# Performance work log

Measured on AMD Instinct MI355X. Metric: run time of the kernel, lower is better.

## Reference

```python
import jax, jax.numpy as jnp
import numpy as np

B, N1, N2 = 8, 2048, 2048
K1D, K2D, V1D, V2D, AD = 256, 256, 256, 256, 128


def setup_inputs() -> dict:
    key = jax.random.key(0)
    ks = jax.random.split(key, 8)
    scale1 = 1.0 / np.sqrt(K1D)
    scale2 = 1.0 / np.sqrt(K2D)
    return {
        "k1": jax.random.normal(ks[0], (B, N1, K1D), jnp.float32),
        "k2": jax.random.normal(ks[1], (B, N2, K2D), jnp.float32),
        "v1": jax.random.normal(ks[2], (B, N1, V1D), jnp.float32),
        "v2": jax.random.normal(ks[3], (B, N2, V2D), jnp.float32),
        "W1": jax.random.uniform(ks[4], (K1D, AD), jnp.float32, -scale1, scale1),
        "b1": jax.random.uniform(ks[5], (AD,), jnp.float32, -scale1, scale1),
        "W2": jax.random.uniform(ks[6], (K2D, AD), jnp.float32, -scale2, scale2),
        "b2": jax.random.uniform(ks[7], (AD,), jnp.float32, -scale2, scale2),
    }


def reference(k1, k2, v1, v2, W1, b1, W2, b2):
    k1p = k1 @ W1 + b1                      # [B, N1, A]
    k2p = k2 @ W2 + b2                      # [B, N2, A]
    score = jnp.einsum("bnd,bmd->bnm", k1p, k2p)   # [B, N1, N2]
    w1 = jax.nn.softmax(score, axis=1)      # softmax over N1 == softmax(score^T, -1)^T
    w2 = jax.nn.softmax(score, axis=-1)     # [B, N1, N2]
    o1 = jnp.einsum("bnm,bnd->bmd", w1, v1)  # [B, N2, V1D]
    o2 = jnp.einsum("bnm,bmd->bnd", w2, v2)  # [B, N1, V2D]
    return (o2, o1)
```

## Files before the change

### kernel.cpp

```cpp
#include <hip/hip_runtime.h>
#include <hip/hip_bf16.h>

#define B_  8
#define N_  2048
#define KD_ 256
#define AD_ 128
#define VD_ 256
#define SQL2E 1.2011224087864498f

using s16x8 = __attribute__((ext_vector_type(8))) short;
using f16x8 = __attribute__((ext_vector_type(8))) _Float16;
using h2    = __attribute__((ext_vector_type(2))) __fp16;
using f32x4 = __attribute__((ext_vector_type(4))) float;

__device__ __forceinline__ f32x4 mfma16(s16x8 a, s16x8 b, f32x4 c) {
  return __builtin_amdgcn_mfma_f32_16x16x32_f16(
      __builtin_bit_cast(f16x8, a), __builtin_bit_cast(f16x8, b), c, 0, 0, 0);
}
__device__ __forceinline__ short f2h(float f) {
  _Float16 h = (_Float16)f;
  return *reinterpret_cast<short*>(&h);
}
__device__ __forceinline__ float exp2_hw(float x) {
#if __has_builtin(__builtin_amdgcn_exp2f)
  return __builtin_amdgcn_exp2f(x);
#else
  float r;
  asm volatile("v_exp_f32 %0, %1" : "=v"(r) : "v"(x));
  return r;
#endif
}
__device__ __forceinline__ s16x8 cvt8(const float* __restrict__ p) {
  union { s16x8 v; h2 h[4]; } u;
  f32x4 a = *(const f32x4*)p;
  f32x4 bq = *(const f32x4*)(p + 4);
  u.h[0] = __builtin_amdgcn_cvt_pkrtz(a[0], a[1]);
  u.h[1] = __builtin_amdgcn_cvt_pkrtz(a[2], a[3]);
  u.h[2] = __builtin_amdgcn_cvt_pkrtz(bq[0], bq[1]);
  u.h[3] = __builtin_amdgcn_cvt_pkrtz(bq[2], bq[3]);
  return u.v;
}

__global__ __launch_bounds__(256) void prep_k(
    const float* __restrict__ k1, const float* __restrict__ k2,
    const float* __restrict__ v1, const float* __restrict__ v2,
    const float* __restrict__ W1, const float* __restrict__ b1f,
    const float* __restrict__ W2, const float* __restrict__ b2f,
    short* __restrict__ q1p, short* __restrict__ q2p,
    short* __restrict__ vt1, short* __restrict__ vt2) {
  __shared__ __align__(16) short sWT[128 * 264];
  const int t  = threadIdx.x;
  const int id = blockIdx.x;

  if (id < 512) {
    const int kt = id & 31, b = (id >> 5) & 7, z = id >> 8;
    const float* src = z ? v2 : v1;
    short*       dst = z ? vt2 : vt1;
    const size_t base = ((size_t)(b * 32 + kt)) * (256 * 64);
    const int w = t >> 6, vchunk = (t >> 4) & 3, l16 = t & 15;
    #pragma unroll
    for (int i = 0; i < 8; i++) {
      float x[8];
      #pragma unroll
      for (int kk = 0; kk < 8; kk++)
        x[kk] = src[((size_t)(b * N_ + kt * 64 + i * 8 + kk)) * VD_ + t];
      union { s16x8 v; h2 h[4]; } u;
      #pragma unroll
      for (int kk = 0; kk < 4; kk++)
        u.h[kk] = __builtin_amdgcn_cvt_pkrtz(x[2 * kk], x[2 * kk + 1]);
      int f = vchunk * 2 + (i >> 2);
      *(s16x8*)&dst[base + (size_t)((w * 8 + f) * 64 + (i & 3) * 16 + l16) * 8] = u.v;
    }
    return;
  }

  const int pid = id - 512;
  const int z = pid >> 8, mb = pid & 255;
  const float* X    = z ? k2 : k1;
  const float* W    = z ? W2 : W1;
  const float* bias = z ? b2f : b1f;
  short*       Y    = z ? q2p : q1p;
  const int m0   = mb * 64;
  const int lane = t & 63, wave = t >> 6, quad = lane >> 4, l16 = lane & 15;

  #pragma unroll
  for (int j = 0; j < 64; j++) {
    int idx = j * 256 + t;
    int n = idx & 127, kh = idx >> 7;
    h2 p = __builtin_amdgcn_cvt_pkrtz(W[(size_t)(2 * kh) * AD_ + n] * SQL2E,
                                      W[(size_t)(2 * kh + 1) * AD_ + n] * SQL2E);
    *(h2*)&sWT[n * 264 + kh * 2] = p;
  }
  const float* xrow = &X[(size_t)(m0 + wave * 16 + l16) * KD_];
  s16x8 a[8];
  #pragma unroll
  for (int ks = 0; ks < 8; ks++) a[ks] = cvt8(xrow + ks * 32 + quad * 8);
  __syncthreads();

  f32x4 acc[8];
  #pragma unroll
  for (int nt = 0; nt < 8; nt++) acc[nt] = (f32x4){0.f, 0.f, 0.f, 0.f};
  #pragma unroll
  for (int ks = 0; ks < 8; ks++) {
    #pragma unroll
    for (int nt = 0; nt < 8; nt++) {
      s16x8 bf = *(const s16x8*)&sWT[(nt * 16 + l16) * 264 + ks * 32 + quad * 8];
      acc[nt] = mfma16(a[ks], bf, acc[nt]);
    }
  }
  #pragma unroll
  for (int nt = 0; nt < 8; nt++) {
    float bv = bias[nt * 16 + l16] * SQL2E;
    #pragma unroll
    for (int r = 0; r < 4; r++) {
      int row = m0 + wave * 16 + quad * 4 + r;
      Y[(size_t)row * AD_ + nt * 16 + l16] = f2h(acc[nt][r] + bv);
    }
  }
}

__global__ __launch_bounds__(256, 2) void attn_k(
    const short* __restrict__ q1p, const short* __restrict__ q2p,
    const short* __restrict__ vt1, const short* __restrict__ vt2,
    float* __restrict__ out) {
  __shared__ __align__(16) short sK[2][64 * 136];
  __shared__ __align__(16) short sP[2][4][16 * 64];
  __shared__ __align__(16) float sAl[2][68];

  const int t    = threadIdx.x;
  const int lane = t & 63, wave = t >> 6, quad = lane >> 4, l16 = lane & 15;
  const int id   = blockIdx.x;
  const int xcd  = id & 7, seq = id >> 3;
  const int bp   = xcd * 2 + (seq >> 5);
  const int qb   = seq & 31;
  const int b    = bp & 7, pass = bp >> 3;
  const int q0   = qb * 64;
  const short* Q  = pass ? q2p : q1p;
  const short* K  = pass ? q1p : q2p;
  const short* Vt = pass ? vt1 : vt2;
  float* O = out + (size_t)pass * ((size_t)B_ * N_ * VD_);

  const short* kp = K + (size_t)(b * N_) * AD_ + (size_t)(t >> 4) * AD_ + (t & 15) * 8;
  const short* vp = Vt + (size_t)b * 32 * (256 * 64) + wave * 4096 + lane * 8;

  s16x8 qf[4];
  #pragma unroll
  for (int ks = 0; ks < 4; ks++)
    qf[ks] = *(const s16x8*)&Q[((size_t)(b * N_ + q0 + wave * 16 + l16)) * AD_ +
                               ks * 32 + quad * 8];

  float m_i = -1e30f, l_i = 0.f;
  f32x4 acc[16];
  #pragma unroll
  for (int c0 = 0; c0 < 16; c0++) acc[c0] = (f32x4){0.f, 0.f, 0.f, 0.f};

  s16x8 pk[4], pv[8];
  auto loadK = [&]() {
    #pragma unroll
    for (int i = 0; i < 4; i++) pk[i] = *(const s16x8*)(kp + i * 16 * AD_);
    kp += 64 * AD_;
  };
  auto loadV = [&]() {
    #pragma unroll
    for (int f = 0; f < 8; f++) pv[f] = *(const s16x8*)(vp + f * 512);
    vp += 256 * 64;
  };
  auto storeK = [&](int cb) {
    #pragma unroll
    for (int i = 0; i < 4; i++) {
      int chunk = i * 256 + t, row = chunk >> 4, c8 = chunk & 15;
      *(s16x8*)&sK[cb][row * 136 + c8 * 8] = pk[i];
    }
  };

  loadK(); storeK(0); loadK(); loadV();
  __syncthreads();

  int c = 0;
  for (int kt = 0; kt < 32; kt++) {
    f32x4 st[4];
    #pragma unroll
    for (int nt = 0; nt < 4; nt++) st[nt] = (f32x4){0.f, 0.f, 0.f, 0.f};
    __builtin_amdgcn_s_setprio(1);
    #pragma unroll
    for (int ks = 0; ks < 4; ks++) {
      #pragma unroll
      for (int nt = 0; nt < 4; nt++) {
        s16x8 kf = *(const s16x8*)&sK[c][(nt * 16 + l16) * 136 + ks * 32 + quad * 8];
        st[nt] = mfma16(kf, qf[ks], st[nt]);
      }
    }
    __builtin_amdgcn_s_setprio(0);

    float c0 = fmaxf(fmaxf(st[0][0], st[1][0]), fmaxf(st[2][0], st[3][0]));
    float c1 = fmaxf(fmaxf(st[0][1], st[1][1]), fmaxf(st[2][1], st[3][1]));
    float c2 = fmaxf(fmaxf(st[0][2], st[1][2]), fmaxf(st[2][2], st[3][2]));
    float c3 = fmaxf(fmaxf(st[0][3], st[1][3]), fmaxf(st[2][3], st[3][3]));
    float mt = fmaxf(fmaxf(c0, c1), fmaxf(c2, c3));
    mt = fmaxf(mt, __shfl_xor(mt, 16));
    mt = fmaxf(mt, __shfl_xor(mt, 32));

    float alpha = 1.f;
    bool  resc  = !__all(mt - m_i <= 8.f);
    if (resc) {
      float mn = fmaxf(m_i, mt);
      alpha = exp2_hw(m_i - mn);
      l_i *= alpha;
      m_i  = mn;
    }

    f32x4 psv = (f32x4){0.f, 0.f, 0.f, 0.f};
    #pragma unroll
    for (int nt = 0; nt < 4; nt++) {
      #pragma unroll
      for (int r = 0; r < 4; r++) {
        float p = exp2_hw(st[nt][r] - m_i);
        st[nt][r] = p;
        psv[r] += p;
      }
    }
    l_i += (psv[0] + psv[1]) + (psv[2] + psv[3]);

    #pragma unroll
    for (int nt = 0; nt < 4; nt++) {
      union { h2 h[2]; uint2 u; } wu;
      wu.h[0] = __builtin_amdgcn_cvt_pkrtz(st[nt][0], st[nt][1]);
      wu.h[1] = __builtin_amdgcn_cvt_pkrtz(st[nt][2], st[nt][3]);
      int cp = (nt * 4 + quad) ^ ((l16 & 7) << 1);
      *(uint2*)&sP[c][wave][l16 * 64 + cp * 4] = wu.u;
    }
    if (quad == 0) sAl[c][wave * 16 + l16] = alpha;
    if (lane == 0) sAl[c][64 + wave] = resc ? 1.f : 0.f;

    if (kt + 1 < 32) storeK(1 - c);

    __syncthreads();

    if (kt + 2 < 32) loadK();

    f32x4 fl = *(const f32x4*)&sAl[c][64];
    if (fl[0] + fl[1] + fl[2] + fl[3] != 0.f) {
      #pragma unroll
      for (int m = 0; m < 4; m++) {
        f32x4 aR = *(const f32x4*)&sAl[c][m * 16 + quad * 4];
        #pragma unroll
        for (int v = 0; v < 4; v++) {
          #pragma unroll
          for (int r = 0; r < 4; r++) acc[m * 4 + v][r] *= aR[r];
        }
      }
    }

    __builtin_amdgcn_s_setprio(1);
    #pragma unroll
    for (int m = 0; m < 4; m++) {
      #pragma unroll
      for (int ks2 = 0; ks2 < 2; ks2++) {
        int cp = (ks2 * 8 + quad * 2) ^ ((l16 & 7) << 1);
        s16x8 af = *(const s16x8*)&sP[c][m][l16 * 64 + cp * 4];
        #pragma unroll
        for (int v = 0; v < 4; v++)
          acc[m * 4 + v] = mfma16(af, pv[v * 2 + ks2], acc[m * 4 + v]);
      }
    }
    __builtin_amdgcn_s_setprio(0);

    if (kt + 1 < 32) loadV();
    c ^= 1;
  }

  float lf = l_i + __shfl_xor(l_i, 16);
  lf += __shfl_xor(lf, 32);
  if (quad == 0) sAl[0][wave * 16 + l16] = lf;
  __syncthreads();
  #pragma unroll
  for (int m = 0; m < 4; m++) {
    f32x4 lv = *(const f32x4*)&sAl[0][m * 16 + quad * 4];
    #pragma unroll
    for (int r = 0; r < 4; r++) {
      float inv = 1.f / lv[r];
      int row = q0 + m * 16 + quad * 4 + r;
      #pragma unroll
      for (int v = 0; v < 4; v++)
        O[((size_t)(b * N_ + row)) * VD_ + wave * 64 + v * 16 + l16] =
            acc[m * 4 + v][r] * inv;
    }
  }
}

extern "C" void kernel_launch(void* const* d_in, const int* in_sizes, int n_in,
                              void* d_out, int out_size, void* d_ws, size_t ws_size,
                              hipStream_t stream) {
  const float* k1 = (const float*)d_in[0];
  const float* k2 = (const float*)d_in[1];
  const float* v1 = (const float*)d_in[2];
  const float* v2 = (const float*)d_in[3];
  const float* W1 = (const float*)d_in[4];
  const float* b1 = (const float*)d_in[5];
  const float* W2 = (const float*)d_in[6];
  const float* b2 = (const float*)d_in[7];

  short* ws  = (short*)d_ws;
  short* q1p = ws;
  short* q2p = q1p + (size_t)16384 * 128;
  short* vt1 = q2p + (size_t)16384 * 128;
  short* vt2 = vt1 + (size_t)B_ * 32 * 256 * 64;
  float* out = (float*)d_out;

  prep_k<<<dim3(1024), dim3(256), 0, stream>>>(k1, k2, v1, v2, W1, b1, W2, b2,
                                               q1p, q2p, vt1, vt2);
  attn_k<<<dim3(512), dim3(256), 0, stream>>>(q1p, q2p, vt1, vt2, out);
}
```

Measured before the change: 180.9 us.

## Halve query tile to 32 rows and split key block across wave pairs

Each block now handles 32 query rows instead of 64, launching twice as many blocks. The four waves are split into two query halves and two key halves, and the row max is exchanged through shared memory. P is shared so each wave accumulates over all 64 keys for half the value columns. Fewer accumulator registers allow launch_bounds of 4 blocks per CU, aiming for higher occupancy. The cost is an extra barrier per iteration, more shared-memory traffic, and K/V tiles being reloaded by twice as many blocks.

New measurement: 219.4 us. +21.3%, slower.

```diff
diff --git a/kernel.cpp b/kernel.cpp
--- a/kernel.cpp
+++ b/kernel.cpp
@@ -119,22 +119,25 @@
   }
 }
 
-__global__ __launch_bounds__(256, 2) void attn_k(
+__global__ __launch_bounds__(256, 4) void attn_k(
     const short* __restrict__ q1p, const short* __restrict__ q2p,
     const short* __restrict__ vt1, const short* __restrict__ vt2,
     float* __restrict__ out) {
   __shared__ __align__(16) short sK[2][64 * 136];
-  __shared__ __align__(16) short sP[2][4][16 * 64];
-  __shared__ __align__(16) float sAl[2][68];
+  __shared__ __align__(16) short sP[4][16 * 40];
+  __shared__ __align__(16) float sM[64];
+  __shared__ __align__(16) float sAl[32];
+  __shared__ __align__(16) float sFl[4];
 
   const int t    = threadIdx.x;
   const int lane = t & 63, wave = t >> 6, quad = lane >> 4, l16 = lane & 15;
+  const int qh   = wave & 1, kh = wave >> 1;
   const int id   = blockIdx.x;
   const int xcd  = id & 7, seq = id >> 3;
-  const int bp   = xcd * 2 + (seq >> 5);
-  const int qb   = seq & 31;
+  const int bp   = xcd * 2 + (seq >> 6);
+  const int qb   = seq & 63;
   const int b    = bp & 7, pass = bp >> 3;
-  const int q0   = qb * 64;
+  const int q0   = qb * 32;
   const short* Q  = pass ? q2p : q1p;
   const short* K  = pass ? q1p : q2p;
   const short* Vt = pass ? vt1 : vt2;
@@ -146,13 +149,13 @@
   s16x8 qf[4];
   #pragma unroll
   for (int ks = 0; ks < 4; ks++)
-    qf[ks] = *(const s16x8*)&Q[((size_t)(b * N_ + q0 + wave * 16 + l16)) * AD_ +
+    qf[ks] = *(const s16x8*)&Q[((size_t)(b * N_ + q0 + qh * 16 + l16)) * AD_ +
                                ks * 32 + quad * 8];
 
   float m_i = -1e30f, l_i = 0.f;
-  f32x4 acc[16];
-  #pragma unroll
-  for (int c0 = 0; c0 < 16; c0++) acc[c0] = (f32x4){0.f, 0.f, 0.f, 0.f};
+  f32x4 acc[8];
+  #pragma unroll
+  for (int c0 = 0; c0 < 8; c0++) acc[c0] = (f32x4){0.f, 0.f, 0.f, 0.f};
 
   s16x8 pk[4], pv[8];
   auto loadK = [&]() {
@@ -176,30 +179,36 @@
   loadK(); storeK(0); loadK(); loadV();
   __syncthreads();
 
-  int c = 0;
   for (int kt = 0; kt < 32; kt++) {
-    f32x4 st[4];
-    #pragma unroll
-    for (int nt = 0; nt < 4; nt++) st[nt] = (f32x4){0.f, 0.f, 0.f, 0.f};
+    const int c = kt & 1;
+    f32x4 st[2];
+    st[0] = (f32x4){0.f, 0.f, 0.f, 0.f};
+    st[1] = (f32x4){0.f, 0.f, 0.f, 0.f};
     __builtin_amdgcn_s_setprio(1);
     #pragma unroll
     for (int ks = 0; ks < 4; ks++) {
       #pragma unroll
-      for (int nt = 0; nt < 4; nt++) {
-        s16x8 kf = *(const s16x8*)&sK[c][(nt * 16 + l16) * 136 + ks * 32 + quad * 8];
+      for (int nt = 0; nt < 2; nt++) {
+        s16x8 kf = *(const s16x8*)&sK[c][(kh * 32 + nt * 16 + l16) * 136 +
+                                         ks * 32 + quad * 8];
         st[nt] = mfma16(kf, qf[ks], st[nt]);
       }
     }
     __builtin_amdgcn_s_setprio(0);
 
-    float c0 = fmaxf(fmaxf(st[0][0], st[1][0]), fmaxf(st[2][0], st[3][0]));
-    float c1 = fmaxf(fmaxf(st[0][1], st[1][1]), fmaxf(st[2][1], st[3][1]));
-    float c2 = fmaxf(fmaxf(st[0][2], st[1][2]), fmaxf(st[2][2], st[3][2]));
-    float c3 = fmaxf(fmaxf(st[0][3], st[1][3]), fmaxf(st[2][3], st[3][3]));
-    float mt = fmaxf(fmaxf(c0, c1), fmaxf(c2, c3));
-    mt = fmaxf(mt, __shfl_xor(mt, 16));
-    mt = fmaxf(mt, __shfl_xor(mt, 32));
-
+    float a0 = fmaxf(st[0][0], st[1][0]), a1 = fmaxf(st[0][1], st[1][1]);
+    float a2 = fmaxf(st[0][2], st[1][2]), a3 = fmaxf(st[0][3], st[1][3]);
+    float hm = fmaxf(fmaxf(a0, a1), fmaxf(a2, a3));
+    hm = fmaxf(hm, __shfl_xor(hm, 16));
+    hm = fmaxf(hm, __shfl_xor(hm, 32));
+    if (quad == 0) sM[wave * 16 + l16] = hm;
+
+    if (kt + 1 < 32) storeK(1 - c);
+    __syncthreads();
+    if (kt + 2 < 32) loadK();
+
+    float pm = sM[(wave ^ 2) * 16 + l16];
+    float mt = fmaxf(hm, pm);
     float alpha = 1.f;
     bool  resc  = !__all(mt - m_i <= 8.f);
     if (resc) {
@@ -208,10 +217,9 @@
       l_i *= alpha;
       m_i  = mn;
     }
-
     f32x4 psv = (f32x4){0.f, 0.f, 0.f, 0.f};
     #pragma unroll
-    for (int nt = 0; nt < 4; nt++) {
+    for (int nt = 0; nt < 2; nt++) {
       #pragma unroll
       for (int r = 0; r < 4; r++) {
         float p = exp2_hw(st[nt][r] - m_i);
@@ -222,27 +230,22 @@
     l_i += (psv[0] + psv[1]) + (psv[2] + psv[3]);
 
     #pragma unroll
-    for (int nt = 0; nt < 4; nt++) {
+    for (int nt = 0; nt < 2; nt++) {
       union { h2 h[2]; uint2 u; } wu;
       wu.h[0] = __builtin_amdgcn_cvt_pkrtz(st[nt][0], st[nt][1]);
       wu.h[1] = __builtin_amdgcn_cvt_pkrtz(st[nt][2], st[nt][3]);
-      int cp = (nt * 4 + quad) ^ ((l16 & 7) << 1);
-      *(uint2*)&sP[c][wave][l16 * 64 + cp * 4] = wu.u;
-    }
-    if (quad == 0) sAl[c][wave * 16 + l16] = alpha;
-    if (lane == 0) sAl[c][64 + wave] = resc ? 1.f : 0.f;
-
-    if (kt + 1 < 32) storeK(1 - c);
-
+      int cpw = (nt * 4 + quad) ^ ((l16 & 3) << 1);
+      *(uint2*)&sP[wave][l16 * 40 + cpw * 4] = wu.u;
+    }
+    if (wave < 2 && quad == 0) sAl[wave * 16 + l16] = alpha;
+    if (wave < 2 && lane == 0) sFl[wave] = resc ? 1.f : 0.f;
     __syncthreads();
 
-    if (kt + 2 < 32) loadK();
-
-    f32x4 fl = *(const f32x4*)&sAl[c][64];
-    if (fl[0] + fl[1] + fl[2] + fl[3] != 0.f) {
-      #pragma unroll
-      for (int m = 0; m < 4; m++) {
-        f32x4 aR = *(const f32x4*)&sAl[c][m * 16 + quad * 4];
+    float f0 = sFl[0], f1 = sFl[1];
+    if (f0 + f1 != 0.f) {
+      #pragma unroll
+      for (int m = 0; m < 2; m++) {
+        f32x4 aR = *(const f32x4*)&sAl[m * 16 + quad * 4];
         #pragma unroll
         for (int v = 0; v < 4; v++) {
           #pragma unroll
@@ -253,11 +256,11 @@
 
     __builtin_amdgcn_s_setprio(1);
     #pragma unroll
-    for (int m = 0; m < 4; m++) {
+    for (int m = 0; m < 2; m++) {
       #pragma unroll
       for (int ks2 = 0; ks2 < 2; ks2++) {
-        int cp = (ks2 * 8 + quad * 2) ^ ((l16 & 7) << 1);
-        s16x8 af = *(const s16x8*)&sP[c][m][l16 * 64 + cp * 4];
+        int cp = (2 * quad) ^ ((l16 & 3) << 1);
+        s16x8 af = *(const s16x8*)&sP[ks2 * 2 + m][l16 * 40 + cp * 4];
         #pragma unroll
         for (int v = 0; v < 4; v++)
           acc[m * 4 + v] = mfma16(af, pv[v * 2 + ks2], acc[m * 4 + v]);
@@ -266,16 +269,18 @@
     __builtin_amdgcn_s_setprio(0);
 
     if (kt + 1 < 32) loadV();
-    c ^= 1;
   }
 
   float lf = l_i + __shfl_xor(l_i, 16);
   lf += __shfl_xor(lf, 32);
-  if (quad == 0) sAl[0][wave * 16 + l16] = lf;
+  if (quad == 0) sM[wave * 16 + l16] = lf;
   __syncthreads();
-  #pragma unroll
-  for (int m = 0; m < 4; m++) {
-    f32x4 lv = *(const f32x4*)&sAl[0][m * 16 + quad * 4];
+  if (wave < 2 && quad == 0)
+    sAl[wave * 16 + l16] = sM[wave * 16 + l16] + sM[(wave + 2) * 16 + l16];
+  __syncthreads();
+  #pragma unroll
+  for (int m = 0; m < 2; m++) {
+    f32x4 lv = *(const f32x4*)&sAl[m * 16 + quad * 4];
     #pragma unroll
     for (int r = 0; r < 4; r++) {
       float inv = 1.f / lv[r];
@@ -309,5 +314,5 @@
 
   prep_k<<<dim3(1024), dim3(256), 0, stream>>>(k1, k2, v1, v2, W1, b1, W2, b2,
                                                q1p, q2p, vt1, vt2);
-  attn_k<<<dim3(512), dim3(256), 0, stream>>>(q1p, q2p, vt1, vt2, out);
-}
+  attn_k<<<dim3(1024), dim3(256), 0, stream>>>(q1p, q2p, vt1, vt2, out);
+}
```

## Split QK^T over key columns per wave and software-pipeline PV across iterations

Applied to the files above, without the earlier changes.

Each wave now loads its own 16-key slice of K straight from global memory into registers and computes scores for all 64 queries, so the shared K tile and its staging stores go away. Row maxima are combined across waves through a small shared buffer. The P·V step for iteration i-1 is deferred and overlapped with the QK^T of iteration i behind a single barrier per iteration. In exchange, each wave holds four times as many Q fragments in registers, does a cross-wave max reduction, and the rescale decision is made per block instead of per wave, which raises register pressure and may hurt occupancy.

Result: no change. 180.6 us, median of 2 (-0.2%).

```diff
diff --git a/kernel.cpp b/kernel.cpp
--- a/kernel.cpp
+++ b/kernel.cpp
@@ -123,9 +123,10 @@
     const short* __restrict__ q1p, const short* __restrict__ q2p,
     const short* __restrict__ vt1, const short* __restrict__ vt2,
     float* __restrict__ out) {
-  __shared__ __align__(16) short sK[2][64 * 136];
-  __shared__ __align__(16) short sP[2][4][16 * 64];
-  __shared__ __align__(16) float sAl[2][68];
+  __shared__ __align__(16) short sP[2][64 * 64];
+  __shared__ __align__(16) float sMt[2][4][16][4];
+  __shared__ __align__(16) float sAl[2][64];
+  __shared__ __align__(16) float sL[64];
 
   const int t    = threadIdx.x;
   const int lane = t & 63, wave = t >> 6, quad = lane >> 4, l16 = lane & 15;
@@ -140,24 +141,27 @@
   const short* Vt = pass ? vt1 : vt2;
   float* O = out + (size_t)pass * ((size_t)B_ * N_ * VD_);
 
-  const short* kp = K + (size_t)(b * N_) * AD_ + (size_t)(t >> 4) * AD_ + (t & 15) * 8;
+  const short* kp = K + ((size_t)(b * N_) + wave * 16 + l16) * AD_ + quad * 8;
   const short* vp = Vt + (size_t)b * 32 * (256 * 64) + wave * 4096 + lane * 8;
 
-  s16x8 qf[4];
-  #pragma unroll
-  for (int ks = 0; ks < 4; ks++)
-    qf[ks] = *(const s16x8*)&Q[((size_t)(b * N_ + q0 + wave * 16 + l16)) * AD_ +
-                               ks * 32 + quad * 8];
-
-  float m_i = -1e30f, l_i = 0.f;
+  s16x8 qf[4][4];
+  #pragma unroll
+  for (int qt = 0; qt < 4; qt++)
+    #pragma unroll
+    for (int ks = 0; ks < 4; ks++)
+      qf[qt][ks] = *(const s16x8*)&Q[((size_t)(b * N_ + q0 + qt * 16 + l16)) * AD_ +
+                                     ks * 32 + quad * 8];
+
+  f32x4 m4 = (f32x4){-1e30f, -1e30f, -1e30f, -1e30f};
+  f32x4 l4 = (f32x4){0.f, 0.f, 0.f, 0.f};
   f32x4 acc[16];
   #pragma unroll
   for (int c0 = 0; c0 < 16; c0++) acc[c0] = (f32x4){0.f, 0.f, 0.f, 0.f};
 
-  s16x8 pk[4], pv[8];
+  s16x8 kf[4], pv[8];
   auto loadK = [&]() {
     #pragma unroll
-    for (int i = 0; i < 4; i++) pk[i] = *(const s16x8*)(kp + i * 16 * AD_);
+    for (int ks = 0; ks < 4; ks++) kf[ks] = *(const s16x8*)(kp + ks * 32);
     kp += 64 * AD_;
   };
   auto loadV = [&]() {
@@ -165,125 +169,145 @@
     for (int f = 0; f < 8; f++) pv[f] = *(const s16x8*)(vp + f * 512);
     vp += 256 * 64;
   };
-  auto storeK = [&](int cb) {
-    #pragma unroll
-    for (int i = 0; i < 4; i++) {
-      int chunk = i * 256 + t, row = chunk >> 4, c8 = chunk & 15;
-      *(s16x8*)&sK[cb][row * 136 + c8 * 8] = pk[i];
-    }
-  };
-
-  loadK(); storeK(0); loadK(); loadV();
+
+  loadK();
+  loadV();
+
+  f32x4 stq[4];
+  bool prevResc = false;
+
+  for (int i = 0; i <= 32; i++) {
+    const int c = i & 1;
+    if (i < 32) {
+      #pragma unroll
+      for (int qt = 0; qt < 4; qt++) stq[qt] = (f32x4){0.f, 0.f, 0.f, 0.f};
+      __builtin_amdgcn_s_setprio(1);
+      #pragma unroll
+      for (int ks = 0; ks < 4; ks++) {
+        #pragma unroll
+        for (int qt = 0; qt < 4; qt++)
+          stq[qt] = mfma16(kf[ks], qf[qt][ks], stq[qt]);
+      }
+      __builtin_amdgcn_s_setprio(0);
+
+      float hm0 = fmaxf(fmaxf(stq[0][0], stq[0][1]), fmaxf(stq[0][2], stq[0][3]));
+      float hm1 = fmaxf(fmaxf(stq[1][0], stq[1][1]), fmaxf(stq[1][2], stq[1][3]));
+      float hm2 = fmaxf(fmaxf(stq[2][0], stq[2][1]), fmaxf(stq[2][2], stq[2][3]));
+      float hm3 = fmaxf(fmaxf(stq[3][0], stq[3][1]), fmaxf(stq[3][2], stq[3][3]));
+      hm0 = fmaxf(hm0, __shfl_xor(hm0, 16)); hm0 = fmaxf(hm0, __shfl_xor(hm0, 32));
+      hm1 = fmaxf(hm1, __shfl_xor(hm1, 16)); hm1 = fmaxf(hm1, __shfl_xor(hm1, 32));
+      hm2 = fmaxf(hm2, __shfl_xor(hm2, 16)); hm2 = fmaxf(hm2, __shfl_xor(hm2, 32));
+      hm3 = fmaxf(hm3, __shfl_xor(hm3, 16)); hm3 = fmaxf(hm3, __shfl_xor(hm3, 32));
+      if (quad == 0) {
+        f32x4 hv = (f32x4){hm0, hm1, hm2, hm3};
+        *(f32x4*)&sMt[c][wave][l16][0] = hv;
+      }
+    }
+
+    __syncthreads();
+    if (i + 1 < 32) loadK();
+
+    if (i > 0) {
+      const int cprev = 1 - c;
+      if (prevResc) {
+        #pragma unroll
+        for (int m = 0; m < 4; m++) {
+          f32x4 aR = *(const f32x4*)&sAl[cprev][m * 16 + quad * 4];
+          #pragma unroll
+          for (int v = 0; v < 4; v++) {
+            #pragma unroll
+            for (int r = 0; r < 4; r++) acc[m * 4 + v][r] *= aR[r];
+          }
+        }
+      }
+      __builtin_amdgcn_s_setprio(1);
+      #pragma unroll
+      for (int m = 0; m < 4; m++) {
+        #pragma unroll
+        for (int ks2 = 0; ks2 < 2; ks2++) {
+          int physr = (ks2 * 8 + quad * 2) ^ ((l16 & 7) << 1);
+          s16x8 af = *(const s16x8*)&sP[cprev][(m * 16 + l16) * 64 + physr * 4];
+          #pragma unroll
+          for (int v = 0; v < 4; v++)
+            acc[m * 4 + v] = mfma16(af, pv[v * 2 + ks2], acc[m * 4 + v]);
+        }
+      }
+      __builtin_amdgcn_s_setprio(0);
+      if (i < 32) loadV();
+    }
+
+    if (i < 32) {
+      f32x4 w0 = *(const f32x4*)&sMt[c][0][l16][0];
+      f32x4 w1 = *(const f32x4*)&sMt[c][1][l16][0];
+      f32x4 w2 = *(const f32x4*)&sMt[c][2][l16][0];
+      f32x4 w3 = *(const f32x4*)&sMt[c][3][l16][0];
+      f32x4 mt4;
+      #pragma unroll
+      for (int qt = 0; qt < 4; qt++)
+        mt4[qt] = fmaxf(fmaxf(w0[qt], w1[qt]), fmaxf(w2[qt], w3[qt]));
+
+      bool ok = (mt4[0] - m4[0] <= 8.f) && (mt4[1] - m4[1] <= 8.f) &&
+                (mt4[2] - m4[2] <= 8.f) && (mt4[3] - m4[3] <= 8.f);
+      bool resc = !__all(ok);
+      if (resc) {
+        f32x4 al;
+        #pragma unroll
+        for (int qt = 0; qt < 4; qt++) {
+          float mn = fmaxf(m4[qt], mt4[qt]);
+          al[qt]  = exp2_hw(m4[qt] - mn);
+          m4[qt]  = mn;
+          l4[qt] *= al[qt];
+        }
+        if (wave == 0 && quad == 0) {
+          #pragma unroll
+          for (int qt = 0; qt < 4; qt++) sAl[c][qt * 16 + l16] = al[qt];
+        }
+      }
+      prevResc = resc;
+
+      #pragma unroll
+      for (int qt = 0; qt < 4; qt++) {
+        float p0 = exp2_hw(stq[qt][0] - m4[qt]);
+        float p1 = exp2_hw(stq[qt][1] - m4[qt]);
+        float p2 = exp2_hw(stq[qt][2] - m4[qt]);
+        float p3 = exp2_hw(stq[qt][3] - m4[qt]);
+        l4[qt] += (p0 + p1) + (p2 + p3);
+        union { h2 h[2]; uint2 u; } wu;
+        wu.h[0] = __builtin_amdgcn_cvt_pkrtz(p0, p1);
+        wu.h[1] = __builtin_amdgcn_cvt_pkrtz(p2, p3);
+        int phys = (wave * 4 + quad) ^ ((l16 & 7) << 1);
+        *(uint2*)&sP[c][(qt * 16 + l16) * 64 + phys * 4] = wu.u;
+      }
+    }
+  }
+
+  #pragma unroll
+  for (int qt = 0; qt < 4; qt++) {
+    l4[qt] += __shfl_xor(l4[qt], 16);
+    l4[qt] += __shfl_xor(l4[qt], 32);
+  }
+  if (quad == 0) *(f32x4*)&sMt[0][wave][l16][0] = l4;
   __syncthreads();
-
-  int c = 0;
-  for (int kt = 0; kt < 32; kt++) {
-    f32x4 st[4];
-    #pragma unroll
-    for (int nt = 0; nt < 4; nt++) st[nt] = (f32x4){0.f, 0.f, 0.f, 0.f};
-    __builtin_amdgcn_s_setprio(1);
-    #pragma unroll
-    for (int ks = 0; ks < 4; ks++) {
-      #pragma unroll
-      for (int nt = 0; nt < 4; nt++) {
-        s16x8 kf = *(const s16x8*)&sK[c][(nt * 16 + l16) * 136 + ks * 32 + quad * 8];
-        st[nt] = mfma16(kf, qf[ks], st[nt]);
-      }
-    }
-    __builtin_amdgcn_s_setprio(0);
-
-    float c0 = fmaxf(fmaxf(st[0][0], st[1][0]), fmaxf(st[2][0], st[3][0]));
-    float c1 = fmaxf(fmaxf(st[0][1], st[1][1]), fmaxf(st[2][1], st[3][1]));
-    float c2 = fmaxf(fmaxf(st[0][2], st[1][2]), fmaxf(st[2][2], st[3][2]));
-    float c3 = fmaxf(fmaxf(st[0][3], st[1][3]), fmaxf(st[2][3], st[3][3]));
-    float mt = fmaxf(fmaxf(c0, c1), fmaxf(c2, c3));
-    mt = fmaxf(mt, __shfl_xor(mt, 16));
-    mt = fmaxf(mt, __shfl_xor(mt, 32));
-
-    float alpha = 1.f;
-    bool  resc  = !__all(mt - m_i <= 8.f);
-    if (resc) {
-      float mn = fmaxf(m_i, mt);
-      alpha = exp2_hw(m_i - mn);
-      l_i *= alpha;
-      m_i  = mn;
-    }
-
-    f32x4 psv = (f32x4){0.f, 0.f, 0.f, 0.f};
-    #pragma unroll
-    for (int nt = 0; nt < 4; nt++) {
-      #pragma unroll
-      for (int r = 0; r < 4; r++) {
-        float p = exp2_hw(st[nt][r] - m_i);
-        st[nt][r] = p;
-        psv[r] += p;
-      }
-    }
-    l_i += (psv[0] + psv[1]) + (psv[2] + psv[3]);
-
-    #pragma unroll
-    for (int nt = 0; nt < 4; nt++) {
-      union { h2 h[2]; uint2 u; } wu;
-      wu.h[0] = __builtin_amdgcn_cvt_pkrtz(st[nt][0], st[nt][1]);
-      wu.h[1] = __builtin_amdgcn_cvt_pkrtz(st[nt][2], st[nt][3]);
-      int cp = (nt * 4 + quad) ^ ((l16 & 7) << 1);
-      *(uint2*)&sP[c][wave][l16 * 64 + cp * 4] = wu.u;
-    }
-    if (quad == 0) sAl[c][wave * 16 + l16] = alpha;
-    if (lane == 0) sAl[c][64 + wave] = resc ? 1.f : 0.f;
-
-    if (kt + 1 < 32) storeK(1 - c);
-
-    __syncthreads();
-
-    if (kt + 2 < 32) loadK();
-
-    f32x4 fl = *(const f32x4*)&sAl[c][64];
-    if (fl[0] + fl[1] + fl[2] + fl[3] != 0.f) {
-      #pragma unroll
-      for (int m = 0; m < 4; m++) {
-        f32x4 aR = *(const f32x4*)&sAl[c][m * 16 + quad * 4];
-        #pragma unroll
-        for (int v = 0; v < 4; v++) {
-          #pragma unroll
-          for (int r = 0; r < 4; r++) acc[m * 4 + v][r] *= aR[r];
-        }
-      }
-    }
-
-    __builtin_amdgcn_s_setprio(1);
-    #pragma unroll
-    for (int m = 0; m < 4; m++) {
-      #pragma unroll
-      for (int ks2 = 0; ks2 < 2; ks2++) {
-        int cp = (ks2 * 8 + quad * 2) ^ ((l16 & 7) << 1);
-        s16x8 af = *(const s16x8*)&sP[c][m][l16 * 64 + cp * 4];
-        #pragma unroll
-        for (int v = 0; v < 4; v++)
-          acc[m * 4 + v] = mfma16(af, pv[v * 2 + ks2], acc[m * 4 + v]);
-      }
-    }
-    __builtin_amdgcn_s_setprio(0);
-
-    if (kt + 1 < 32) loadV();
-    c ^= 1;
-  }
-
-  float lf = l_i + __shfl_xor(l_i, 16);
-  lf += __shfl_xor(lf, 32);
-  if (quad == 0) sAl[0][wave * 16 + l16] = lf;
+  if (wave == 0 && quad == 0) {
+    f32x4 s0 = *(const f32x4*)&sMt[0][0][l16][0];
+    f32x4 s1 = *(const f32x4*)&sMt[0][1][l16][0];
+    f32x4 s2 = *(const f32x4*)&sMt[0][2][l16][0];
+    f32x4 s3 = *(const f32x4*)&sMt[0][3][l16][0];
+    #pragma unroll
+    for (int qt = 0; qt < 4; qt++)
+      sL[qt * 16 + l16] = 1.f / (s0[qt] + s1[qt] + s2[qt] + s3[qt]);
+  }
   __syncthreads();
   #pragma unroll
   for (int m = 0; m < 4; m++) {
-    f32x4 lv = *(const f32x4*)&sAl[0][m * 16 + quad * 4];
+    f32x4 lv = *(const f32x4*)&sL[m * 16 + quad * 4];
     #pragma unroll
     for (int r = 0; r < 4; r++) {
-      float inv = 1.f / lv[r];
       int row = q0 + m * 16 + quad * 4 + r;
       #pragma unroll
       for (int v = 0; v < 4; v++)
         O[((size_t)(b * N_ + row)) * VD_ + wave * 64 + v * 16 + l16] =
-            acc[m * 4 + v][r] * inv;
+            acc[m * 4 + v][r] * lv[r];
     }
   }
 }
```

## Load K fragments directly from global into registers, dropping LDS staging

Applied to the files above, without the earlier changes.

Removes the shared-memory double buffer for the K tile. Each wave now loads its full set of MFMA K fragments (16 x 8 halves per lane) straight from global memory into registers, prefetching the next tile right after the QK MFMAs. This cuts the LDS store/read traffic and its bank pressure. The cost is that every wave fetches the whole K tile redundantly (4x global/L2 reads) and register pressure rises by 64 VGPRs, which could hurt occupancy at launch_bounds(256,2).

Result: slower. 254.4 us (+40.7%).

```diff
diff --git a/kernel.cpp b/kernel.cpp
--- a/kernel.cpp
+++ b/kernel.cpp
@@ -123,7 +123,6 @@
     const short* __restrict__ q1p, const short* __restrict__ q2p,
     const short* __restrict__ vt1, const short* __restrict__ vt2,
     float* __restrict__ out) {
-  __shared__ __align__(16) short sK[2][64 * 136];
   __shared__ __align__(16) short sP[2][4][16 * 64];
   __shared__ __align__(16) float sAl[2][68];
 
@@ -140,7 +139,7 @@
   const short* Vt = pass ? vt1 : vt2;
   float* O = out + (size_t)pass * ((size_t)B_ * N_ * VD_);
 
-  const short* kp = K + (size_t)(b * N_) * AD_ + (size_t)(t >> 4) * AD_ + (t & 15) * 8;
+  const short* kp = K + ((size_t)(b * N_) + l16) * AD_ + quad * 8;
   const short* vp = Vt + (size_t)b * 32 * (256 * 64) + wave * 4096 + lane * 8;
 
   s16x8 qf[4];
@@ -154,10 +153,13 @@
   #pragma unroll
   for (int c0 = 0; c0 < 16; c0++) acc[c0] = (f32x4){0.f, 0.f, 0.f, 0.f};
 
-  s16x8 pk[4], pv[8];
-  auto loadK = [&]() {
-    #pragma unroll
-    for (int i = 0; i < 4; i++) pk[i] = *(const s16x8*)(kp + i * 16 * AD_);
+  s16x8 kf[16], pv[8];
+  auto loadK16 = [&]() {
+    #pragma unroll
+    for (int x = 0; x < 16; x++) {
+      int ks = x >> 2, nt = x & 3;
+      kf[x] = *(const s16x8*)(kp + (size_t)(nt * 16) * AD_ + ks * 32);
+    }
     kp += 64 * AD_;
   };
   auto loadV = [&]() {
@@ -165,16 +167,9 @@
     for (int f = 0; f < 8; f++) pv[f] = *(const s16x8*)(vp + f * 512);
     vp += 256 * 64;
   };
-  auto storeK = [&](int cb) {
-    #pragma unroll
-    for (int i = 0; i < 4; i++) {
-      int chunk = i * 256 + t, row = chunk >> 4, c8 = chunk & 15;
-      *(s16x8*)&sK[cb][row * 136 + c8 * 8] = pk[i];
-    }
-  };
-
-  loadK(); storeK(0); loadK(); loadV();
-  __syncthreads();
+
+  loadK16();
+  loadV();
 
   int c = 0;
   for (int kt = 0; kt < 32; kt++) {
@@ -183,14 +178,11 @@
     for (int nt = 0; nt < 4; nt++) st[nt] = (f32x4){0.f, 0.f, 0.f, 0.f};
     __builtin_amdgcn_s_setprio(1);
     #pragma unroll
-    for (int ks = 0; ks < 4; ks++) {
-      #pragma unroll
-      for (int nt = 0; nt < 4; nt++) {
-        s16x8 kf = *(const s16x8*)&sK[c][(nt * 16 + l16) * 136 + ks * 32 + quad * 8];
-        st[nt] = mfma16(kf, qf[ks], st[nt]);
-      }
-    }
+    for (int x = 0; x < 16; x++)
+      st[x & 3] = mfma16(kf[x], qf[x >> 2], st[x & 3]);
     __builtin_amdgcn_s_setprio(0);
+
+    if (kt + 1 < 32) loadK16();
 
     float c0 = fmaxf(fmaxf(st[0][0], st[1][0]), fmaxf(st[2][0], st[3][0]));
     float c1 = fmaxf(fmaxf(st[0][1], st[1][1]), fmaxf(st[2][1], st[3][1]));
@@ -232,11 +224,7 @@
     if (quad == 0) sAl[c][wave * 16 + l16] = alpha;
     if (lane == 0) sAl[c][64 + wave] = resc ? 1.f : 0.f;
 
-    if (kt + 1 < 32) storeK(1 - c);
-
     __syncthreads();
-
-    if (kt + 2 < 32) loadK();
 
     f32x4 fl = *(const f32x4*)&sAl[c][64];
     if (fl[0] + fl[1] + fl[2] + fl[3] != 0.f) {
```
